# Kernel tuning notes

Measured on AMD Instinct MI355X. Metric: run time of the kernel, lower is better.

## Reference

```python
import jax, jax.numpy as jnp
import numpy as np

NU, NI, D = 100000, 50000, 128
N = NU + NI
E = 1500000
L = 8  # padded words per text field
HALF = D // 2


def setup_inputs() -> dict:
    key = jax.random.key(0)
    ks = jax.random.split(key, 24)
    rn = lambda k, s, sc=0.05: jax.random.normal(k, s, dtype=jnp.float32) * sc
    inp = {
        'edge_index': jax.random.randint(ks[0], (2, E), 0, N, dtype=jnp.int32),
        'user_features': jax.random.randint(ks[1], (NU, 10), 0, 5000, dtype=jnp.int32),
        'item_features': jax.random.randint(ks[2], (NI, 10), 0, 8000, dtype=jnp.int32),
        'user_text': jax.random.randint(ks[3], (NU, 3, L), 0, 30000, dtype=jnp.int32),
        'item_text': jax.random.randint(ks[4], (NI, 3, L), 0, 30000, dtype=jnp.int32),
        'user_id_emb': rn(ks[5], (NU, D), 1.0),
        'item_id_emb': rn(ks[6], (NI, D), 1.0),
        'user_feat_emb': rn(ks[7], (5000, D)),
        'item_feat_emb': rn(ks[8], (8000, D)),
        'word_emb': rn(ks[9], (30000, HALF)),
        'user_projW': rn(ks[10], (2 * D + HALF * 3 - D, D)) if False else rn(ks[10], (320, D)),
        'user_projb': jnp.zeros((D,), jnp.float32),
        'item_projW': rn(ks[11], (320, D)),
        'item_projb': jnp.zeros((D,), jnp.float32),
        'w0W': rn(ks[12], (2 * D, D)),
        'w0b': jnp.zeros((D,), jnp.float32),
        'w1W': rn(ks[13], (2 * D, D)),
        'w1b': jnp.zeros((D,), jnp.float32),
        'v0W': rn(ks[14], (D, D)),
        'v0b': jnp.zeros((D,), jnp.float32),
        'v1W': rn(ks[15], (D, D)),
        'v1b': jnp.zeros((D,), jnp.float32),
    }
    return inp


def reference(edge_index, user_features, item_features, user_text, item_text,
              user_id_emb, item_id_emb, user_feat_emb, item_feat_emb, word_emb,
              user_projW, user_projb, item_projW, item_projb,
              w0W, w0b, w1W, w1b, v0W, v0b, v1W, v1b):
    # --- initial node embeddings: multi-table gather + mean + concat + proj ---
    def text_embedding(text_idx):
        # [n,3,L] word ids -> mean word emb per field -> concat -> [n, 3*HALF]
        te = word_emb[text_idx].mean(axis=2)  # [n,3,HALF]
        return te.reshape(te.shape[0], -1)

    u_text = text_embedding(user_text)                       # [NU, 1.5D]
    i_text = text_embedding(item_text)                       # [NI, 1.5D]
    u_feat = user_feat_emb[user_features].mean(axis=1)       # [NU, D]
    i_feat = item_feat_emb[item_features].mean(axis=1)       # [NI, D]
    u0 = jnp.concatenate([u_feat, u_text], axis=1) @ user_projW + user_projb
    i0 = jnp.concatenate([i_feat, i_text], axis=1) @ item_projW + item_projb
    x = jnp.concatenate([u0 + user_id_emb, i0 + item_id_emb], axis=0)  # [N, D]

    # --- SAGE layers: gather-by-src, segment-mean-by-dst, concat, linear ---
    src, dst = edge_index[0], edge_index[1]
    deg = jnp.maximum(jax.ops.segment_sum(jnp.ones((E,), x.dtype), dst, num_segments=N), 1.0)
    layers = [(w0W, w0b, v0W, v0b, False), (w1W, w1b, v1W, v1b, True)]
    for wW, wb, vW, vb, last in layers:
        agg = jax.ops.segment_sum(x[src], dst, num_segments=N) / deg[:, None]  # mean neighbor
        agg = jax.nn.relu(agg @ vW + vb)
        x = jnp.concatenate([x, agg], axis=1) @ wW + wb
        if not last:
            x = jax.nn.relu(x)
    return x  # [N, D]: rows [0,NU) users, [NU,N) items
```

## Files before the change

### kernel.cpp

```cpp
#include <hip/hip_runtime.h>

#define D 128
#define HALF 64
constexpr int INB = 32;

typedef __attribute__((ext_vector_type(8))) short short8;
typedef __attribute__((ext_vector_type(4))) float f32x4;
typedef unsigned short u16;
typedef unsigned int u32;

__device__ __forceinline__ u16 f2b(float f) {
    u32 u = __builtin_bit_cast(u32, f);
    u32 r = (u + 0x7fffu + ((u >> 16) & 1u)) >> 16;
    return (u16)r;
}
__device__ __forceinline__ float b2f_lo(u32 v) { return __builtin_bit_cast(float, v << 16); }
__device__ __forceinline__ float b2f_hi(u32 v) { return __builtin_bit_cast(float, v & 0xffff0000u); }

#define MFMA __builtin_amdgcn_mfma_f32_16x16x32_bf16

__global__ __launch_bounds__(256) void transpose_bf16_kernel(
    const float* __restrict__ in, u16* __restrict__ out, int K, int N)
{
    int idx = blockIdx.x * 256 + threadIdx.x;
    if (idx >= K * N) return;
    int k = idx / N, n = idx % N;
    out[(size_t)n * K + k] = f2b(in[idx]);
}

__global__ __launch_bounds__(256) void init_mfma_kernel(
    const int* __restrict__ feat_ids,
    const int* __restrict__ text_ids,
    const float* __restrict__ feat_emb,
    const float* __restrict__ word_emb,
    const u16* __restrict__ Pt,
    const float* __restrict__ projb,
    const float* __restrict__ id_emb,
    u16* __restrict__ xb,
    int n_nodes, int out_base)
{
    __shared__ u16 in_s[INB][328];
    __shared__ int fid_s[INB][10];
    __shared__ int tid_s[INB][24];
    const int base = blockIdx.x * INB;
    const int t = threadIdx.x;

    for (int i = t; i < INB * 10; i += 256) {
        int node = i / 10, j = i % 10;
        int g = base + node; if (g > n_nodes - 1) g = n_nodes - 1;
        fid_s[node][j] = feat_ids[(size_t)g * 10 + j];
    }
    for (int i = t; i < INB * 24; i += 256) {
        int node = i / 24, j = i % 24;
        int g = base + node; if (g > n_nodes - 1) g = n_nodes - 1;
        tid_s[node][j] = text_ids[(size_t)g * 24 + j];
    }
    __syncthreads();

    for (int i = t; i < INB * 128; i += 256) {
        int node = i >> 7, d = i & 127;
        float acc = 0.f;
        #pragma unroll
        for (int j = 0; j < 10; ++j) acc += feat_emb[(size_t)fid_s[node][j] * D + d];
        in_s[node][d] = f2b(acc * 0.1f);
    }
    for (int i = t; i < INB * 192; i += 256) {
        int node = i / 192, tt = i % 192;
        int f = tt >> 6, d2 = tt & 63;
        float acc = 0.f;
        #pragma unroll
        for (int w = 0; w < 8; ++w) acc += word_emb[(size_t)tid_s[node][f * 8 + w] * HALF + d2];
        in_s[node][128 + tt] = f2b(acc * 0.125f);
    }
    __syncthreads();

    const int wid = t >> 6, lane = t & 63;
    const int row16 = lane & 15, kq = lane >> 4;
    const int g2 = wid >> 1;
    const int oh = wid & 1;
    const int lnode = g2 * 16 + row16;
    const int node = base + lnode;

    short8 Bfrag[10];
    #pragma unroll
    for (int kk = 0; kk < 10; ++kk)
        Bfrag[kk] = *(const short8*)&in_s[lnode][kk * 32 + kq * 8];

    #pragma unroll
    for (int fp = 0; fp < 4; ++fp) {
        const int fn = oh * 4 + fp;
        f32x4 c = {0.f, 0.f, 0.f, 0.f};
        #pragma unroll
        for (int kk = 0; kk < 10; ++kk) {
            short8 A = *(const short8*)&Pt[(size_t)(fn * 16 + row16) * 320 + kk * 32 + kq * 8];
            c = MFMA(A, Bfrag[kk], c, 0, 0, 0);
        }
        if (node < n_nodes) {
            float4 bv = *(const float4*)&projb[fn * 16 + kq * 4];
            float4 ie = *(const float4*)&id_emb[(size_t)node * D + fn * 16 + kq * 4];
            ushort4 ow;
            ow.x = f2b(c[0] + bv.x + ie.x);
            ow.y = f2b(c[1] + bv.y + ie.y);
            ow.z = f2b(c[2] + bv.z + ie.z);
            ow.w = f2b(c[3] + bv.w + ie.w);
            *(ushort4*)&xb[(size_t)(out_base + node) * D + fn * 16 + kq * 4] = ow;
        }
    }
}

__global__ __launch_bounds__(256) void hist_kernel(
    const int* __restrict__ dst, int E, int* __restrict__ deg)
{
    int e = blockIdx.x * 256 + threadIdx.x;
    if (e < E) atomicAdd(&deg[dst[e]], 1);
}

__global__ __launch_bounds__(256) void scan1_kernel(
    const int* __restrict__ deg, int n, int* __restrict__ out_ex, int* __restrict__ bsums)
{
    __shared__ int s[256];
    const int t = threadIdx.x;
    const int base = blockIdx.x * 1024 + t * 4;
    int v0 = 0, v1 = 0, v2 = 0, v3 = 0;
    if (base + 0 < n) v0 = deg[base + 0];
    if (base + 1 < n) v1 = deg[base + 1];
    if (base + 2 < n) v2 = deg[base + 2];
    if (base + 3 < n) v3 = deg[base + 3];
    int sum = v0 + v1 + v2 + v3;
    s[t] = sum;
    __syncthreads();
    for (int off = 1; off < 256; off <<= 1) {
        int tmp = (t >= off) ? s[t - off] : 0;
        __syncthreads();
        s[t] += tmp;
        __syncthreads();
    }
    int ex = s[t] - sum;
    if (t == 255) bsums[blockIdx.x] = s[255];
    if (base + 0 < n) out_ex[base + 0] = ex;
    if (base + 1 < n) out_ex[base + 1] = ex + v0;
    if (base + 2 < n) out_ex[base + 2] = ex + v0 + v1;
    if (base + 3 < n) out_ex[base + 3] = ex + v0 + v1 + v2;
}

__global__ __launch_bounds__(256) void scan2_kernel(int* __restrict__ bsums, int nb)
{
    __shared__ int s[256];
    const int t = threadIdx.x;
    int v = (t < nb) ? bsums[t] : 0;
    s[t] = v;
    __syncthreads();
    for (int off = 1; off < 256; off <<= 1) {
        int tmp = (t >= off) ? s[t - off] : 0;
        __syncthreads();
        s[t] += tmp;
        __syncthreads();
    }
    if (t < nb) bsums[t] = s[t] - v;
}

__global__ __launch_bounds__(256) void scan3_kernel(
    int* __restrict__ row_ptr, const int* __restrict__ bsums, int n, int E)
{
    const int add = bsums[blockIdx.x];
    const int base = blockIdx.x * 1024 + threadIdx.x * 4;
    #pragma unroll
    for (int j = 0; j < 4; ++j)
        if (base + j < n) row_ptr[base + j] += add;
    if (blockIdx.x == 0 && threadIdx.x == 0) row_ptr[n] = E;
}

__global__ __launch_bounds__(256) void fill_kernel(
    const int* __restrict__ src, const int* __restrict__ dst, int E,
    const int* __restrict__ row_ptr, int* __restrict__ cursor, int* __restrict__ ebuf)
{
    int e = blockIdx.x * 256 + threadIdx.x;
    if (e < E) {
        int d = dst[e];
        int slot = atomicAdd(&cursor[d], 1);
        ebuf[row_ptr[d] + slot] = src[e];
    }
}

__global__ __launch_bounds__(256) void aggregate_kernel(
    const int* __restrict__ row_ptr, const int* __restrict__ ebuf,
    const u16* __restrict__ xb, u16* __restrict__ aggm, int n_nodes)
{
    const int wave = threadIdx.x >> 6;
    const int lane = threadIdx.x & 63;
    const int g = blockIdx.x * 4 + wave;
    if (g >= n_nodes) return;
    const int s0 = row_ptr[g], s1 = row_ptr[g + 1];
    float ax = 0.f, ay = 0.f;
    for (int e = s0; e < s1; ++e) {
        int s = ebuf[e];
        u32 v = *(const u32*)&xb[(size_t)s * D + lane * 2];
        ax += b2f_lo(v);
        ay += b2f_hi(v);
    }
    const float inv = 1.0f / fmaxf((float)(s1 - s0), 1.0f);
    u32 o = (u32)f2b(ax * inv) | ((u32)f2b(ay * inv) << 16);
    *(u32*)&aggm[(size_t)g * D + lane * 2] = o;
}

__global__ __launch_bounds__(512, 4) void sage_mfma_kernel(
    const u16* __restrict__ xb, const u16* __restrict__ aggm,
    const u16* __restrict__ Vt,  const float* __restrict__ vb,
    const u16* __restrict__ Wt,  const float* __restrict__ wb,
    u16* __restrict__ xb_out,
    float* __restrict__ f_out,
    int n_nodes)
{
    __shared__ u16 t_lds[32][136];
    const int wid  = threadIdx.x >> 6;
    const int lane = threadIdx.x & 63;
    const int row16 = lane & 15;
    const int kq    = lane >> 4;
    const int nb = blockIdx.x * 32;

    const int node0 = nb + row16;
    const int node1 = nb + 16 + row16;
    const int ncl0 = node0 < n_nodes ? node0 : n_nodes - 1;
    const int ncl1 = node1 < n_nodes ? node1 : n_nodes - 1;

    short8 Av[4];
    #pragma unroll
    for (int kk = 0; kk < 4; ++kk)
        Av[kk] = *(const short8*)&Vt[(size_t)(wid * 16 + row16) * 128 + kk * 32 + kq * 8];

    #pragma unroll
    for (int g = 0; g < 2; ++g) {
        const int nclamp = g ? ncl1 : ncl0;
        f32x4 c = {0.f, 0.f, 0.f, 0.f};
        #pragma unroll
        for (int kk = 0; kk < 4; ++kk) {
            short8 B = *(const short8*)&aggm[(size_t)nclamp * D + kk * 32 + kq * 8];
            c = MFMA(Av[kk], B, c, 0, 0, 0);
        }
        float4 bv = *(const float4*)&vb[wid * 16 + kq * 4];
        ushort4 tw;
        tw.x = f2b(fmaxf(c[0] + bv.x, 0.f));
        tw.y = f2b(fmaxf(c[1] + bv.y, 0.f));
        tw.z = f2b(fmaxf(c[2] + bv.z, 0.f));
        tw.w = f2b(fmaxf(c[3] + bv.w, 0.f));
        *(ushort4*)&t_lds[g * 16 + row16][wid * 16 + kq * 4] = tw;
    }

    short8 Aw[8];
    #pragma unroll
    for (int kk = 0; kk < 8; ++kk)
        Aw[kk] = *(const short8*)&Wt[(size_t)(wid * 16 + row16) * 256 + kk * 32 + kq * 8];

    short8 Bx0[4], Bx1[4];
    #pragma unroll
    for (int kk = 0; kk < 4; ++kk)
        Bx0[kk] = *(const short8*)&xb[(size_t)ncl0 * D + kk * 32 + kq * 8];
    #pragma unroll
    for (int kk = 0; kk < 4; ++kk)
        Bx1[kk] = *(const short8*)&xb[(size_t)ncl1 * D + kk * 32 + kq * 8];

    __syncthreads();

    #pragma unroll
    for (int g = 0; g < 2; ++g) {
        const int node = g ? node1 : node0;
        f32x4 c = {0.f, 0.f, 0.f, 0.f};
        #pragma unroll
        for (int kk = 0; kk < 4; ++kk)
            c = MFMA(Aw[kk], g ? Bx1[kk] : Bx0[kk], c, 0, 0, 0);
        #pragma unroll
        for (int kk = 0; kk < 4; ++kk) {
            short8 B = *(const short8*)&t_lds[g * 16 + row16][kk * 32 + kq * 8];
            c = MFMA(Aw[4 + kk], B, c, 0, 0, 0);
        }
        if (node < n_nodes) {
            float4 bv = *(const float4*)&wb[wid * 16 + kq * 4];
            float o0 = c[0] + bv.x, o1 = c[1] + bv.y, o2 = c[2] + bv.z, o3 = c[3] + bv.w;
            if (xb_out) {
                ushort4 ow;
                ow.x = f2b(fmaxf(o0, 0.f));
                ow.y = f2b(fmaxf(o1, 0.f));
                ow.z = f2b(fmaxf(o2, 0.f));
                ow.w = f2b(fmaxf(o3, 0.f));
                *(ushort4*)&xb_out[(size_t)node * D + wid * 16 + kq * 4] = ow;
            } else {
                float4 ow = make_float4(o0, o1, o2, o3);
                *(float4*)&f_out[(size_t)node * D + wid * 16 + kq * 4] = ow;
            }
        }
    }
}

extern "C" void kernel_launch(void* const* d_in, const int* in_sizes, int n_in,
                              void* d_out, int out_size, void* d_ws, size_t ws_size,
                              hipStream_t stream)
{
    const int* edge_index      = (const int*)d_in[0];
    const int* user_features   = (const int*)d_in[1];
    const int* item_features   = (const int*)d_in[2];
    const int* user_text       = (const int*)d_in[3];
    const int* item_text       = (const int*)d_in[4];
    const float* user_id_emb   = (const float*)d_in[5];
    const float* item_id_emb   = (const float*)d_in[6];
    const float* user_feat_emb = (const float*)d_in[7];
    const float* item_feat_emb = (const float*)d_in[8];
    const float* word_emb      = (const float*)d_in[9];
    const float* user_projW    = (const float*)d_in[10];
    const float* user_projb    = (const float*)d_in[11];
    const float* item_projW    = (const float*)d_in[12];
    const float* item_projb    = (const float*)d_in[13];
    const float* w0W = (const float*)d_in[14];
    const float* w0b = (const float*)d_in[15];
    const float* w1W = (const float*)d_in[16];
    const float* w1b = (const float*)d_in[17];
    const float* v0W = (const float*)d_in[18];
    const float* v0b = (const float*)d_in[19];
    const float* v1W = (const float*)d_in[20];
    const float* v1b = (const float*)d_in[21];

    const int E  = in_sizes[0] / 2;
    const int NU = in_sizes[5] / D;
    const int NI = in_sizes[6] / D;
    const int N  = NU + NI;
    const int NB = (N + 1023) / 1024;

    u16* xb   = (u16*)d_ws;
    u16* aggm = xb + (size_t)N * D;
    u16* Vt0  = aggm + (size_t)N * D;
    u16* Vt1  = Vt0 + 128 * 128;
    u16* Wt0  = Vt1 + 128 * 128;
    u16* Wt1  = Wt0 + 256 * 128;
    u16* Pt_u = Wt1 + 256 * 128;
    u16* Pt_i = Pt_u + 128 * 320;
    int* row_ptr = (int*)(Pt_i + 128 * 320);
    int* deg_i   = row_ptr + (N + 1);
    int* cursor  = deg_i + N;
    int* bsums   = cursor + N;
    int* ebuf    = bsums + 256;

    hipMemsetAsync(deg_i, 0, (size_t)(2 * N) * sizeof(int), stream);

    const int* src = edge_index;
    const int* dst = edge_index + E;
    dim3 blk(256);

    transpose_bf16_kernel<<<(128 * 128 + 255) / 256, blk, 0, stream>>>(v0W, Vt0, 128, 128);
    transpose_bf16_kernel<<<(128 * 128 + 255) / 256, blk, 0, stream>>>(v1W, Vt1, 128, 128);
    transpose_bf16_kernel<<<(256 * 128 + 255) / 256, blk, 0, stream>>>(w0W, Wt0, 256, 128);
    transpose_bf16_kernel<<<(256 * 128 + 255) / 256, blk, 0, stream>>>(w1W, Wt1, 256, 128);
    transpose_bf16_kernel<<<(320 * 128 + 255) / 256, blk, 0, stream>>>(user_projW, Pt_u, 320, 128);
    transpose_bf16_kernel<<<(320 * 128 + 255) / 256, blk, 0, stream>>>(item_projW, Pt_i, 320, 128);

    init_mfma_kernel<<<(NU + INB - 1) / INB, blk, 0, stream>>>(
        user_features, user_text, user_feat_emb, word_emb,
        Pt_u, user_projb, user_id_emb, xb, NU, 0);
    init_mfma_kernel<<<(NI + INB - 1) / INB, blk, 0, stream>>>(
        item_features, item_text, item_feat_emb, word_emb,
        Pt_i, item_projb, item_id_emb, xb, NI, NU);

    hist_kernel<<<(E + 255) / 256, blk, 0, stream>>>(dst, E, deg_i);
    scan1_kernel<<<NB, blk, 0, stream>>>(deg_i, N, row_ptr, bsums);
    scan2_kernel<<<1, blk, 0, stream>>>(bsums, NB);
    scan3_kernel<<<NB, blk, 0, stream>>>(row_ptr, bsums, N, E);
    fill_kernel<<<(E + 255) / 256, blk, 0, stream>>>(src, dst, E, row_ptr, cursor, ebuf);

    const int sage_grid = (N + 31) / 32;
    dim3 sblk(512);

    aggregate_kernel<<<(N + 3) / 4, blk, 0, stream>>>(row_ptr, ebuf, xb, aggm, N);
    sage_mfma_kernel<<<sage_grid, sblk, 0, stream>>>(
        xb, aggm, Vt0, v0b, Wt0, w0b, xb, nullptr, N);

    aggregate_kernel<<<(N + 3) / 4, blk, 0, stream>>>(row_ptr, ebuf, xb, aggm, N);
    sage_mfma_kernel<<<sage_grid, sblk, 0, stream>>>(
        xb, aggm, Vt1, v1b, Wt1, w1b, nullptr, (float*)d_out, N);
}
```

Measured before the change: 1.077 ms.

## Convert embedding tables to bf16, merge launches, unroll neighbor aggregation

Fuses the six weight-transpose launches into one kernel and the user/item init launches into one. Adds a pass that converts the feature and word embedding tables to bf16 so the init gathers move half the bytes, using vectorized 8-byte loads. Unrolls the aggregation loop by four to keep more independent gathers in flight. The cost is an extra conversion pass plus workspace for the bf16 tables, and one more rounding of the embeddings before they are averaged.

```diff
diff --git a/kernel.cpp b/kernel.cpp
--- a/kernel.cpp
+++ b/kernel.cpp
@@ -19,30 +19,72 @@
 
 #define MFMA __builtin_amdgcn_mfma_f32_16x16x32_bf16
 
-__global__ __launch_bounds__(256) void transpose_bf16_kernel(
-    const float* __restrict__ in, u16* __restrict__ out, int K, int N)
-{
-    int idx = blockIdx.x * 256 + threadIdx.x;
-    if (idx >= K * N) return;
-    int k = idx / N, n = idx % N;
+__global__ __launch_bounds__(256) void transpose_all_kernel(
+    const float* __restrict__ v0W, const float* __restrict__ v1W,
+    const float* __restrict__ w0W, const float* __restrict__ w1W,
+    const float* __restrict__ pu,  const float* __restrict__ pi,
+    u16* __restrict__ Vt0, u16* __restrict__ Vt1,
+    u16* __restrict__ Wt0, u16* __restrict__ Wt1,
+    u16* __restrict__ Ptu, u16* __restrict__ Pti)
+{
+    int i = blockIdx.x * 256 + threadIdx.x;
+    const float* in; u16* out; int K, idx;
+    if      (i <  16384) { in = v0W; out = Vt0; K = 128; idx = i; }
+    else if (i <  32768) { in = v1W; out = Vt1; K = 128; idx = i - 16384; }
+    else if (i <  65536) { in = w0W; out = Wt0; K = 256; idx = i - 32768; }
+    else if (i <  98304) { in = w1W; out = Wt1; K = 256; idx = i - 65536; }
+    else if (i < 139264) { in = pu;  out = Ptu; K = 320; idx = i - 98304; }
+    else if (i < 180224) { in = pi;  out = Pti; K = 320; idx = i - 139264; }
+    else return;
+    int k = idx >> 7, n = idx & 127;
     out[(size_t)n * K + k] = f2b(in[idx]);
 }
 
+__global__ __launch_bounds__(256) void convert_tables_kernel(
+    const float* __restrict__ a, int na,
+    const float* __restrict__ b, int nb_,
+    const float* __restrict__ c, int nc,
+    u16* __restrict__ oa, u16* __restrict__ ob, u16* __restrict__ oc)
+{
+    int total = (na + nb_ + nc) >> 2;
+    for (int i = blockIdx.x * 256 + threadIdx.x; i < total; i += gridDim.x * 256) {
+        int idx = i << 2;
+        const float* src; u16* dst; int off;
+        if (idx < na)            { src = a; dst = oa; off = idx; }
+        else if (idx < na + nb_) { src = b; dst = ob; off = idx - na; }
+        else                     { src = c; dst = oc; off = idx - na - nb_; }
+        float4 v = *(const float4*)&src[off];
+        ushort4 o;
+        o.x = f2b(v.x); o.y = f2b(v.y); o.z = f2b(v.z); o.w = f2b(v.w);
+        *(ushort4*)&dst[off] = o;
+    }
+}
+
 __global__ __launch_bounds__(256) void init_mfma_kernel(
-    const int* __restrict__ feat_ids,
-    const int* __restrict__ text_ids,
-    const float* __restrict__ feat_emb,
-    const float* __restrict__ word_emb,
-    const u16* __restrict__ Pt,
-    const float* __restrict__ projb,
-    const float* __restrict__ id_emb,
+    const int* __restrict__ ufeat, const int* __restrict__ utext,
+    const u16* __restrict__ ufb,   const u16* __restrict__ uPt,
+    const float* __restrict__ upb, const float* __restrict__ uid,
+    const int* __restrict__ ifeat, const int* __restrict__ itext,
+    const u16* __restrict__ ifb,   const u16* __restrict__ iPt,
+    const float* __restrict__ ipb, const float* __restrict__ iid,
+    const u16* __restrict__ word_b,
     u16* __restrict__ xb,
-    int n_nodes, int out_base)
+    int NU, int NI, int ublocks)
 {
     __shared__ u16 in_s[INB][328];
     __shared__ int fid_s[INB][10];
     __shared__ int tid_s[INB][24];
-    const int base = blockIdx.x * INB;
+
+    const bool isU = (int)blockIdx.x < ublocks;
+    const int* feat_ids = isU ? ufeat : ifeat;
+    const int* text_ids = isU ? utext : itext;
+    const u16* feat_b   = isU ? ufb   : ifb;
+    const u16* Pt       = isU ? uPt   : iPt;
+    const float* projb  = isU ? upb   : ipb;
+    const float* id_emb = isU ? uid   : iid;
+    const int n_nodes   = isU ? NU    : NI;
+    const int out_base  = isU ? 0     : NU;
+    const int base = (isU ? blockIdx.x : blockIdx.x - ublocks) * INB;
     const int t = threadIdx.x;
 
     for (int i = t; i < INB * 10; i += 256) {
@@ -57,20 +99,34 @@
     }
     __syncthreads();
 
-    for (int i = t; i < INB * 128; i += 256) {
-        int node = i >> 7, d = i & 127;
-        float acc = 0.f;
-        #pragma unroll
-        for (int j = 0; j < 10; ++j) acc += feat_emb[(size_t)fid_s[node][j] * D + d];
-        in_s[node][d] = f2b(acc * 0.1f);
-    }
-    for (int i = t; i < INB * 192; i += 256) {
-        int node = i / 192, tt = i % 192;
-        int f = tt >> 6, d2 = tt & 63;
-        float acc = 0.f;
-        #pragma unroll
-        for (int w = 0; w < 8; ++w) acc += word_emb[(size_t)tid_s[node][f * 8 + w] * HALF + d2];
-        in_s[node][128 + tt] = f2b(acc * 0.125f);
+    for (int i = t; i < INB * 32; i += 256) {
+        int node = i >> 5, dq = i & 31;
+        float a0 = 0.f, a1 = 0.f, a2 = 0.f, a3 = 0.f;
+        #pragma unroll
+        for (int j = 0; j < 10; ++j) {
+            uint2 v = *(const uint2*)&feat_b[(size_t)fid_s[node][j] * D + dq * 4];
+            a0 += b2f_lo(v.x); a1 += b2f_hi(v.x);
+            a2 += b2f_lo(v.y); a3 += b2f_hi(v.y);
+        }
+        ushort4 o;
+        o.x = f2b(a0 * 0.1f); o.y = f2b(a1 * 0.1f);
+        o.z = f2b(a2 * 0.1f); o.w = f2b(a3 * 0.1f);
+        *(ushort4*)&in_s[node][dq * 4] = o;
+    }
+    for (int i = t; i < INB * 48; i += 256) {
+        int node = i / 48, r = i % 48;
+        int f = r >> 4, dq = r & 15;
+        float a0 = 0.f, a1 = 0.f, a2 = 0.f, a3 = 0.f;
+        #pragma unroll
+        for (int w = 0; w < 8; ++w) {
+            uint2 v = *(const uint2*)&word_b[(size_t)tid_s[node][f * 8 + w] * HALF + dq * 4];
+            a0 += b2f_lo(v.x); a1 += b2f_hi(v.x);
+            a2 += b2f_lo(v.y); a3 += b2f_hi(v.y);
+        }
+        ushort4 o;
+        o.x = f2b(a0 * 0.125f); o.y = f2b(a1 * 0.125f);
+        o.z = f2b(a2 * 0.125f); o.w = f2b(a3 * 0.125f);
+        *(ushort4*)&in_s[node][128 + f * 64 + dq * 4] = o;
     }
     __syncthreads();
 
@@ -191,13 +247,25 @@
     const int g = blockIdx.x * 4 + wave;
     if (g >= n_nodes) return;
     const int s0 = row_ptr[g], s1 = row_ptr[g + 1];
-    float ax = 0.f, ay = 0.f;
-    for (int e = s0; e < s1; ++e) {
-        int s = ebuf[e];
-        u32 v = *(const u32*)&xb[(size_t)s * D + lane * 2];
+    float ax = 0.f, ay = 0.f, bx = 0.f, by = 0.f;
+    int e = s0;
+    for (; e + 4 <= s1; e += 4) {
+        int n0 = ebuf[e], n1 = ebuf[e + 1], n2 = ebuf[e + 2], n3 = ebuf[e + 3];
+        u32 v0 = *(const u32*)&xb[(size_t)n0 * D + lane * 2];
+        u32 v1 = *(const u32*)&xb[(size_t)n1 * D + lane * 2];
+        u32 v2 = *(const u32*)&xb[(size_t)n2 * D + lane * 2];
+        u32 v3 = *(const u32*)&xb[(size_t)n3 * D + lane * 2];
+        ax += b2f_lo(v0) + b2f_lo(v1);
+        ay += b2f_hi(v0) + b2f_hi(v1);
+        bx += b2f_lo(v2) + b2f_lo(v3);
+        by += b2f_hi(v2) + b2f_hi(v3);
+    }
+    for (; e < s1; ++e) {
+        u32 v = *(const u32*)&xb[(size_t)ebuf[e] * D + lane * 2];
         ax += b2f_lo(v);
         ay += b2f_hi(v);
     }
+    ax += bx; ay += by;
     const float inv = 1.0f / fmaxf((float)(s1 - s0), 1.0f);
     u32 o = (u32)f2b(ax * inv) | ((u32)f2b(ay * inv) << 16);
     *(u32*)&aggm[(size_t)g * D + lane * 2] = o;
@@ -323,6 +391,9 @@
     const int NI = in_sizes[6] / D;
     const int N  = NU + NI;
     const int NB = (N + 1023) / 1024;
+    const int nFU = in_sizes[7];
+    const int nFI = in_sizes[8];
+    const int nW  = in_sizes[9];
 
     u16* xb   = (u16*)d_ws;
     u16* aggm = xb + (size_t)N * D;
@@ -332,7 +403,10 @@
     u16* Wt1  = Wt0 + 256 * 128;
     u16* Pt_u = Wt1 + 256 * 128;
     u16* Pt_i = Pt_u + 128 * 320;
-    int* row_ptr = (int*)(Pt_i + 128 * 320);
+    u16* fb_u = Pt_i + 128 * 320;
+    u16* fb_i = fb_u + (size_t)nFU;
+    u16* wd_b = fb_i + (size_t)nFI;
+    int* row_ptr = (int*)(wd_b + (size_t)nW);
     int* deg_i   = row_ptr + (N + 1);
     int* cursor  = deg_i + N;
     int* bsums   = cursor + N;
@@ -344,19 +418,19 @@
     const int* dst = edge_index + E;
     dim3 blk(256);
 
-    transpose_bf16_kernel<<<(128 * 128 + 255) / 256, blk, 0, stream>>>(v0W, Vt0, 128, 128);
-    transpose_bf16_kernel<<<(128 * 128 + 255) / 256, blk, 0, stream>>>(v1W, Vt1, 128, 128);
-    transpose_bf16_kernel<<<(256 * 128 + 255) / 256, blk, 0, stream>>>(w0W, Wt0, 256, 128);
-    transpose_bf16_kernel<<<(256 * 128 + 255) / 256, blk, 0, stream>>>(w1W, Wt1, 256, 128);
-    transpose_bf16_kernel<<<(320 * 128 + 255) / 256, blk, 0, stream>>>(user_projW, Pt_u, 320, 128);
-    transpose_bf16_kernel<<<(320 * 128 + 255) / 256, blk, 0, stream>>>(item_projW, Pt_i, 320, 128);
-
-    init_mfma_kernel<<<(NU + INB - 1) / INB, blk, 0, stream>>>(
-        user_features, user_text, user_feat_emb, word_emb,
-        Pt_u, user_projb, user_id_emb, xb, NU, 0);
-    init_mfma_kernel<<<(NI + INB - 1) / INB, blk, 0, stream>>>(
-        item_features, item_text, item_feat_emb, word_emb,
-        Pt_i, item_projb, item_id_emb, xb, NI, NU);
+    transpose_all_kernel<<<(180224 + 255) / 256, blk, 0, stream>>>(
+        v0W, v1W, w0W, w1W, user_projW, item_projW,
+        Vt0, Vt1, Wt0, Wt1, Pt_u, Pt_i);
+    convert_tables_kernel<<<2048, blk, 0, stream>>>(
+        user_feat_emb, nFU, item_feat_emb, nFI, word_emb, nW,
+        fb_u, fb_i, wd_b);
+
+    const int ublocks = (NU + INB - 1) / INB;
+    const int iblocks = (NI + INB - 1) / INB;
+    init_mfma_kernel<<<ublocks + iblocks, blk, 0, stream>>>(
+        user_features, user_text, fb_u, Pt_u, user_projb, user_id_emb,
+        item_features, item_text, fb_i, Pt_i, item_projb, item_id_emb,
+        wd_b, xb, NU, NI, ublocks);
 
     hist_kernel<<<(E + 255) / 256, blk, 0, stream>>>(dst, E, deg_i);
     scan1_kernel<<<NB, blk, 0, stream>>>(deg_i, N, row_ptr, bsums);
```

Result: faster. 881.3 us (-18.2%).
